# Optimization experiments

Measured on AMD Instinct MI355X. Metric: run time of the kernel, lower is better.

## Reference

```python
import jax, jax.numpy as jnp
import numpy as np

N = 100000      # nodes
E = 1600000     # edges (avg degree 16)
F_IN = 256
F_OUT = 128


def setup_inputs() -> dict:
    key = jax.random.key(0)
    k1, k2, k3, k4, k5 = jax.random.split(key, 5)
    x = jax.random.normal(k1, (N, F_IN), dtype=jnp.float32)
    adj_row = jax.random.randint(k2, (E,), 0, N, dtype=jnp.int32)
    adj_col = jax.random.randint(k3, (E,), 0, N, dtype=jnp.int32)
    adj_vals = jax.random.uniform(k4, (E,), dtype=jnp.float32)
    # he_uniform init for weight, zeros for bias (as in build())
    limit = jnp.sqrt(6.0 / F_IN)
    w = jax.random.uniform(k5, (F_IN, F_OUT), minval=-limit, maxval=limit, dtype=jnp.float32)
    b = jnp.zeros((F_OUT,), dtype=jnp.float32)
    return {"x": x, "adj_row": adj_row, "adj_col": adj_col, "adj_vals": adj_vals, "w": w, "b": b}


def reference(x, adj_row, adj_col, adj_vals, w, b):
    # dense feature transform: [N, F_in] @ [F_in, F_out] -> [N, F_out]
    h = x @ w
    # sparse adjacency SpMM (COO): out[r] += vals[e] * h[c] for edge e=(r,c)
    msgs = adj_vals[:, None] * h[adj_col]            # [E, F_out]
    agg = jax.ops.segment_sum(msgs, adj_row, num_segments=N)  # [N, F_out]
    # bias + relu activation
    return jax.nn.relu(agg + b)
```

## Files before the change

kernel.cpp:

```cpp
#include <hip/hip_runtime.h>
#include <hip/hip_bf16.h>
#include <cstdint>
#include <cstddef>

#define N_NODES 100000
#define N_EDGES 1600000
#define F_IN 256
#define F_OUT 128

#define NB 782
#define NBLK 196
#define TILE 8192
#define CAP 4096

typedef __attribute__((ext_vector_type(8))) short short8;
typedef __attribute__((ext_vector_type(4))) float floatx4;

static __device__ __forceinline__ unsigned short f2bf(float f) {
    union { float f; unsigned u; } v; v.f = f;
    unsigned r = v.u + 0x7FFF + ((v.u >> 16) & 1);
    return (unsigned short)(r >> 16);
}

__global__ void prep_w(const float* __restrict__ w, unsigned short* __restrict__ wT) {
    int i = blockIdx.x * 256 + threadIdx.x;
    int k = i >> 7;
    int n = i & 127;
    int g = (k >> 3) ^ (n & 7);
    wT[n * 256 + g * 8 + (k & 7)] = f2bf(w[i]);
}

__global__ __launch_bounds__(256, 2) void gemm_xw(const float* __restrict__ x,
                                                  const unsigned short* __restrict__ wT,
                                                  unsigned short* __restrict__ h) {
    __shared__ __align__(16) unsigned short wlds[128 * 256];
    const int tid = threadIdx.x;
    {
        const floatx4* src = reinterpret_cast<const floatx4*>(wT);
        floatx4* dst = reinterpret_cast<floatx4*>(wlds);
        #pragma unroll
        for (int i = 0; i < 16; i++) dst[tid + i * 256] = src[tid + i * 256];
    }
    __syncthreads();

    const int wave = tid >> 6, lane = tid & 63;
    const int quad = lane >> 4, l16 = lane & 15;
    const int rowbase = blockIdx.x * 256 + wave * 64;

    floatx4 acc[4][8];
    #pragma unroll
    for (int mf = 0; mf < 4; mf++)
        #pragma unroll
        for (int nt = 0; nt < 8; nt++) acc[mf][nt] = (floatx4)0.f;

    #pragma unroll
    for (int ks = 0; ks < 8; ks++) {
        const int k0 = ks * 32 + quad * 8;
        short8 afrag[4];
        #pragma unroll
        for (int mf = 0; mf < 4; mf++) {
            int row = rowbase + mf * 16 + l16;
            if (row >= N_NODES) row = N_NODES - 1;
            const float* xp = x + (size_t)row * F_IN + k0;
            floatx4 x0 = *reinterpret_cast<const floatx4*>(xp);
            floatx4 x1 = *reinterpret_cast<const floatx4*>(xp + 4);
            short8 a;
            a[0] = (short)f2bf(x0[0]); a[1] = (short)f2bf(x0[1]);
            a[2] = (short)f2bf(x0[2]); a[3] = (short)f2bf(x0[3]);
            a[4] = (short)f2bf(x1[0]); a[5] = (short)f2bf(x1[1]);
            a[6] = (short)f2bf(x1[2]); a[7] = (short)f2bf(x1[3]);
            afrag[mf] = a;
        }
        short8 bfrag[8];
        const int gq = ks * 4 + quad;
        #pragma unroll
        for (int nt = 0; nt < 8; nt++) {
            const int n = nt * 16 + l16;
            const int g = gq ^ (n & 7);
            bfrag[nt] = *reinterpret_cast<const short8*>(&wlds[n * 256 + g * 8]);
        }
        #pragma unroll
        for (int mf = 0; mf < 4; mf++)
            #pragma unroll
            for (int nt = 0; nt < 8; nt++)
                acc[mf][nt] = __builtin_amdgcn_mfma_f32_16x16x32_bf16(
                    afrag[mf], bfrag[nt], acc[mf][nt], 0, 0, 0);
    }

    #pragma unroll
    for (int mf = 0; mf < 4; mf++) {
        const int mbase = rowbase + mf * 16 + quad * 4;
        #pragma unroll
        for (int reg = 0; reg < 4; reg++) {
            const int m = mbase + reg;
            if (m < N_NODES) {
                #pragma unroll
                for (int nt = 0; nt < 8; nt++)
                    h[(size_t)m * F_OUT + nt * 16 + l16] = f2bf(acc[mf][nt][reg]);
            }
        }
    }
}

__global__ __launch_bounds__(256) void bucket_hist(const int* __restrict__ row,
                                                   int* __restrict__ bucket_total,
                                                   int* __restrict__ blockbase) {
    __shared__ int hist[NB];
    const int t = threadIdx.x, blk = blockIdx.x;
    for (int i = t; i < NB; i += 256) hist[i] = 0;
    __syncthreads();
    const long tb = (long)blk * TILE;
    #pragma unroll
    for (int c = 0; c < 8; c++) {
        long i0 = tb + c * 1024 + t * 4;
        if (i0 + 4 <= N_EDGES) {
            int4 r = *reinterpret_cast<const int4*>(row + i0);
            atomicAdd(&hist[r.x >> 7], 1); atomicAdd(&hist[r.y >> 7], 1);
            atomicAdd(&hist[r.z >> 7], 1); atomicAdd(&hist[r.w >> 7], 1);
        } else {
            for (long i = i0; i < N_EDGES && i < i0 + 4; i++)
                atomicAdd(&hist[row[i] >> 7], 1);
        }
    }
    __syncthreads();
    for (int bin = t; bin < NB; bin += 256)
        blockbase[bin * NBLK + blk] = atomicAdd(&bucket_total[bin], hist[bin]);
}

__global__ void bucket_scan(const int* __restrict__ bucket_total,
                            int* __restrict__ bucket_base) {
    __shared__ int sm[1024];
    const int t = threadIdx.x;
    int v = (t < NB) ? bucket_total[t] : 0;
    sm[t] = v; __syncthreads();
    for (int off = 1; off < 1024; off <<= 1) {
        int x2 = (t >= off) ? sm[t - off] : 0;
        __syncthreads();
        sm[t] += x2;
        __syncthreads();
    }
    if (t < NB) bucket_base[t] = sm[t] - v;
    if (t == NB - 1) bucket_base[NB] = sm[t];
}

__global__ __launch_bounds__(256) void bucket_scatter(const int* __restrict__ row,
                                                      const int* __restrict__ col,
                                                      const float* __restrict__ val,
                                                      const int* __restrict__ bucket_base,
                                                      const int* __restrict__ blockbase,
                                                      int2* __restrict__ metabuf) {
    __shared__ int sbase[NB];
    const int t = threadIdx.x, blk = blockIdx.x;
    for (int bin = t; bin < NB; bin += 256)
        sbase[bin] = bucket_base[bin] + blockbase[bin * NBLK + blk];
    __syncthreads();
    const long tb = (long)blk * TILE;
    #pragma unroll
    for (int c = 0; c < 8; c++) {
        long i0 = tb + c * 1024 + t * 4;
        if (i0 + 4 <= N_EDGES) {
            int4 r  = *reinterpret_cast<const int4*>(row + i0);
            int4 cc = *reinterpret_cast<const int4*>(col + i0);
            floatx4 vv = *reinterpret_cast<const floatx4*>(val + i0);
            int rr[4] = {r.x, r.y, r.z, r.w};
            int c4[4] = {cc.x, cc.y, cc.z, cc.w};
            float v4[4] = {vv[0], vv[1], vv[2], vv[3]};
            #pragma unroll
            for (int j = 0; j < 4; j++) {
                int bin = rr[j] >> 7, rl = rr[j] & 127;
                int pos = atomicAdd(&sbase[bin], 1);
                metabuf[pos] = make_int2(c4[j] | (rl << 24), __float_as_int(v4[j]));
            }
        } else {
            for (long i = i0; i < N_EDGES && i < i0 + 4; i++) {
                int rv = row[i];
                int bin = rv >> 7, rl = rv & 127;
                int pos = atomicAdd(&sbase[bin], 1);
                metabuf[pos] = make_int2(col[i] | (rl << 24), __float_as_int(val[i]));
            }
        }
    }
}

__global__ __launch_bounds__(512, 8) void spmm_fused(const unsigned short* __restrict__ h,
                                                     const int* __restrict__ bucket_base,
                                                     const int2* __restrict__ meta,
                                                     const float* __restrict__ bias,
                                                     float* __restrict__ out) {
    __shared__ int2 st[CAP];
    __shared__ int hist[128], scanb[128], startS[128], cursor[128];
    const int t = threadIdx.x, b = blockIdx.x;
    const int b0 = bucket_base[b];
    int n = bucket_base[b + 1] - b0; if (n > CAP) n = CAP;

    if (t < 128) hist[t] = 0;
    __syncthreads();
    for (int i = t; i < n; i += 512)
        atomicAdd(&hist[((unsigned)meta[b0 + i].x >> 24) & 127], 1);
    __syncthreads();
    if (t < 128) scanb[t] = hist[t];
    __syncthreads();
    for (int off = 1; off < 128; off <<= 1) {
        int v = (t >= off && t < 128) ? scanb[t - off] : 0;
        __syncthreads();
        if (t < 128) scanb[t] += v;
        __syncthreads();
    }
    if (t < 128) { int e = scanb[t] - hist[t]; startS[t] = e; cursor[t] = e; }
    __syncthreads();
    for (int i = t; i < n; i += 512) {
        int2 e = meta[b0 + i];
        int rl = ((unsigned)e.x >> 24) & 127;
        int pos = atomicAdd(&cursor[rl], 1);
        st[pos] = make_int2(e.x & 0x00FFFFFF, e.y);
    }
    __syncthreads();

    const int lane = t & 63;
    const int l16 = lane & 15;
    const int grp = (t >> 6) * 4 + (lane >> 4);
    const unsigned short* hp = h + l16 * 8;
    const floatx4 bv0 = *reinterpret_cast<const floatx4*>(bias + l16 * 8);
    const floatx4 bv1 = *reinterpret_cast<const floatx4*>(bias + l16 * 8 + 4);

    #pragma unroll
    for (int j = 0; j < 4; j++) {
        const int rl = grp * 4 + j;
        const int s = startS[rl], d = hist[rl];
        float acc[8];
        #pragma unroll
        for (int k = 0; k < 8; k++) acc[k] = 0.f;
        for (int i = 0; i < d; i += 4) {
            int2 mm[4];
            #pragma unroll
            for (int u = 0; u < 4; u++) {
                int idx = i + u; if (idx > d - 1) idx = d - 1;
                mm[u] = st[s + idx];
            }
            uint4 hv[4];
            #pragma unroll
            for (int u = 0; u < 4; u++)
                hv[u] = *reinterpret_cast<const uint4*>(hp + (size_t)mm[u].x * F_OUT);
            #pragma unroll
            for (int u = 0; u < 4; u++) {
                float v = (i + u < d) ? __int_as_float(mm[u].y) : 0.f;
                #pragma unroll
                for (int k = 0; k < 4; k++) {
                    unsigned uu = ((const unsigned*)&hv[u])[k];
                    acc[2 * k]     += v * __uint_as_float(uu << 16);
                    acc[2 * k + 1] += v * __uint_as_float(uu & 0xffff0000u);
                }
            }
        }
        const int r = b * 128 + rl;
        if (r < N_NODES) {
            floatx4 o0, o1;
            #pragma unroll
            for (int k = 0; k < 4; k++) o0[k] = fmaxf(acc[k] + bv0[k], 0.f);
            #pragma unroll
            for (int k = 0; k < 4; k++) o1[k] = fmaxf(acc[4 + k] + bv1[k], 0.f);
            float* op = out + (size_t)r * F_OUT + l16 * 8;
            *reinterpret_cast<floatx4*>(op) = o0;
            *reinterpret_cast<floatx4*>(op + 4) = o1;
        }
    }
}

extern "C" void kernel_launch(void* const* d_in, const int* in_sizes, int n_in,
                              void* d_out, int out_size, void* d_ws, size_t ws_size,
                              hipStream_t stream) {
    const float* x        = (const float*)d_in[0];
    const int*   adj_row  = (const int*)d_in[1];
    const int*   adj_col  = (const int*)d_in[2];
    const float* adj_vals = (const float*)d_in[3];
    const float* w        = (const float*)d_in[4];
    const float* b        = (const float*)d_in[5];
    float* out = (float*)d_out;

    char* ws = (char*)d_ws;
    unsigned short* wT = (unsigned short*)ws;
    unsigned short* h  = (unsigned short*)(ws + 65536);
    size_t off = 65536 + (size_t)N_NODES * F_OUT * 2;
    int2* metabuf  = (int2*)(ws + off);   off += (size_t)N_EDGES * 8;
    int* blockbase = (int*)(ws + off);    off += (size_t)NB * NBLK * 4;
    int* bucket_total = (int*)(ws + off); off += 3136;
    int* bucket_base  = (int*)(ws + off); off += 3136;

    prep_w<<<128, 256, 0, stream>>>(w, wT);
    hipMemsetAsync(bucket_total, 0, NB * 4, stream);
    gemm_xw<<<(N_NODES + 255) / 256, 256, 0, stream>>>(x, wT, h);
    bucket_hist<<<NBLK, 256, 0, stream>>>(adj_row, bucket_total, blockbase);
    bucket_scan<<<1, 1024, 0, stream>>>(bucket_total, bucket_base);
    bucket_scatter<<<NBLK, 256, 0, stream>>>(adj_row, adj_col, adj_vals,
                                             bucket_base, blockbase, metabuf);
    spmm_fused<<<NB, 512, 0, stream>>>(h, bucket_base, metabuf, b, out);
}
```

Measured before the change: 305.8 us.

## Vectorize h stores, use wave-shuffle scans, and prefetch SpMM gathers

The GEMM now writes each row's eight bf16 outputs as one 16-byte store, so h is kept in a column-interleaved layout. SpMM un-permutes that layout when it writes its output, using strided scalar stores and per-element bias loads. Both prefix scans, the global bucket scan and the per-block row-histogram scan, are replaced by 64-lane shuffle scans, which removes many barriers. The SpMM gather loop is software-pipelined: the next four neighbour rows are loaded while the current four are accumulated, at the cost of higher register pressure.

```diff
diff --git a/kernel.cpp b/kernel.cpp
--- a/kernel.cpp
+++ b/kernel.cpp
@@ -94,9 +94,10 @@
         for (int reg = 0; reg < 4; reg++) {
             const int m = mbase + reg;
             if (m < N_NODES) {
+                short8 hv;
                 #pragma unroll
-                for (int nt = 0; nt < 8; nt++)
-                    h[(size_t)m * F_OUT + nt * 16 + l16] = f2bf(acc[mf][nt][reg]);
+                for (int nt = 0; nt < 8; nt++) hv[nt] = (short)f2bf(acc[mf][nt][reg]);
+                *reinterpret_cast<short8*>(&h[(size_t)m * F_OUT + l16 * 8]) = hv;
             }
         }
     }
@@ -129,18 +130,27 @@
 
 __global__ void bucket_scan(const int* __restrict__ bucket_total,
                             int* __restrict__ bucket_base) {
-    __shared__ int sm[1024];
-    const int t = threadIdx.x;
-    int v = (t < NB) ? bucket_total[t] : 0;
-    sm[t] = v; __syncthreads();
-    for (int off = 1; off < 1024; off <<= 1) {
-        int x2 = (t >= off) ? sm[t - off] : 0;
-        __syncthreads();
-        sm[t] += x2;
-        __syncthreads();
-    }
-    if (t < NB) bucket_base[t] = sm[t] - v;
-    if (t == NB - 1) bucket_base[NB] = sm[t];
+    const int lane = threadIdx.x;
+    int loc[13];
+    int s = 0;
+    #pragma unroll
+    for (int k = 0; k < 13; k++) {
+        int idx = lane * 13 + k;
+        int v = (idx < NB) ? bucket_total[idx] : 0;
+        loc[k] = s; s += v;
+    }
+    int run = s;
+    #pragma unroll
+    for (int off = 1; off < 64; off <<= 1) {
+        int u = __shfl_up(run, off);
+        if (lane >= off) run += u;
+    }
+    const int base = run - s;
+    #pragma unroll
+    for (int k = 0; k < 13; k++) {
+        int idx = lane * 13 + k;
+        if (idx <= NB) bucket_base[idx] = base + loc[k];
+    }
 }
 
 __global__ __launch_bounds__(256) void bucket_scatter(const int* __restrict__ row,
@@ -188,7 +198,7 @@
                                                      const float* __restrict__ bias,
                                                      float* __restrict__ out) {
     __shared__ int2 st[CAP];
-    __shared__ int hist[128], scanb[128], startS[128], cursor[128];
+    __shared__ int hist[128], startS[128], cursor[128];
     const int t = threadIdx.x, b = blockIdx.x;
     const int b0 = bucket_base[b];
     int n = bucket_base[b + 1] - b0; if (n > CAP) n = CAP;
@@ -198,15 +208,19 @@
     for (int i = t; i < n; i += 512)
         atomicAdd(&hist[((unsigned)meta[b0 + i].x >> 24) & 127], 1);
     __syncthreads();
-    if (t < 128) scanb[t] = hist[t];
-    __syncthreads();
-    for (int off = 1; off < 128; off <<= 1) {
-        int v = (t >= off && t < 128) ? scanb[t - off] : 0;
-        __syncthreads();
-        if (t < 128) scanb[t] += v;
-        __syncthreads();
-    }
-    if (t < 128) { int e = scanb[t] - hist[t]; startS[t] = e; cursor[t] = e; }
+    if (t < 64) {
+        int h0 = hist[t], h1 = hist[t + 64];
+        int s0 = h0, s1 = h1;
+        #pragma unroll
+        for (int off = 1; off < 64; off <<= 1) {
+            int u0 = __shfl_up(s0, off);
+            int u1 = __shfl_up(s1, off);
+            if (t >= off) { s0 += u0; s1 += u1; }
+        }
+        s1 += __shfl(s0, 63);
+        startS[t] = s0 - h0;      cursor[t] = s0 - h0;
+        startS[t + 64] = s1 - h1; cursor[t + 64] = s1 - h1;
+    }
     __syncthreads();
     for (int i = t; i < n; i += 512) {
         int2 e = meta[b0 + i];
@@ -220,8 +234,6 @@
     const int l16 = lane & 15;
     const int grp = (t >> 6) * 4 + (lane >> 4);
     const unsigned short* hp = h + l16 * 8;
-    const floatx4 bv0 = *reinterpret_cast<const floatx4*>(bias + l16 * 8);
-    const floatx4 bv1 = *reinterpret_cast<const floatx4*>(bias + l16 * 8 + 4);
 
     #pragma unroll
     for (int j = 0; j < 4; j++) {
@@ -230,38 +242,52 @@
         float acc[8];
         #pragma unroll
         for (int k = 0; k < 8; k++) acc[k] = 0.f;
-        for (int i = 0; i < d; i += 4) {
-            int2 mm[4];
-            #pragma unroll
-            for (int u = 0; u < 4; u++) {
-                int idx = i + u; if (idx > d - 1) idx = d - 1;
-                mm[u] = st[s + idx];
-            }
-            uint4 hv[4];
+        if (d > 0) {
+            int2 mmc[4];
+            uint4 hvc[4];
+            #pragma unroll
+            for (int u = 0; u < 4; u++) { int idx = (u < d) ? u : d - 1; mmc[u] = st[s + idx]; }
             #pragma unroll
             for (int u = 0; u < 4; u++)
-                hv[u] = *reinterpret_cast<const uint4*>(hp + (size_t)mm[u].x * F_OUT);
-            #pragma unroll
-            for (int u = 0; u < 4; u++) {
-                float v = (i + u < d) ? __int_as_float(mm[u].y) : 0.f;
+                hvc[u] = *reinterpret_cast<const uint4*>(hp + (size_t)mmc[u].x * F_OUT);
+            for (int i = 0; i < d; i += 4) {
+                int2 mmn[4];
+                uint4 hvn[4];
+                const bool more = (i + 4) < d;
+                if (more) {
+                    #pragma unroll
+                    for (int u = 0; u < 4; u++) {
+                        int idx = i + 4 + u; if (idx > d - 1) idx = d - 1;
+                        mmn[u] = st[s + idx];
+                    }
+                    #pragma unroll
+                    for (int u = 0; u < 4; u++)
+                        hvn[u] = *reinterpret_cast<const uint4*>(hp + (size_t)mmn[u].x * F_OUT);
+                }
                 #pragma unroll
-                for (int k = 0; k < 4; k++) {
-                    unsigned uu = ((const unsigned*)&hv[u])[k];
-                    acc[2 * k]     += v * __uint_as_float(uu << 16);
-                    acc[2 * k + 1] += v * __uint_as_float(uu & 0xffff0000u);
+                for (int u = 0; u < 4; u++) {
+                    float v = (i + u < d) ? __int_as_float(mmc[u].y) : 0.f;
+                    #pragma unroll
+                    for (int k = 0; k < 4; k++) {
+                        unsigned uu = ((const unsigned*)&hvc[u])[k];
+                        acc[2 * k]     += v * __uint_as_float(uu << 16);
+                        acc[2 * k + 1] += v * __uint_as_float(uu & 0xffff0000u);
+                    }
+                }
+                if (more) {
+                    #pragma unroll
+                    for (int u = 0; u < 4; u++) { mmc[u] = mmn[u]; hvc[u] = hvn[u]; }
                 }
             }
         }
         const int r = b * 128 + rl;
         if (r < N_NODES) {
-            floatx4 o0, o1;
-            #pragma unroll
-            for (int k = 0; k < 4; k++) o0[k] = fmaxf(acc[k] + bv0[k], 0.f);
-            #pragma unroll
-            for (int k = 0; k < 4; k++) o1[k] = fmaxf(acc[4 + k] + bv1[k], 0.f);
-            float* op = out + (size_t)r * F_OUT + l16 * 8;
-            *reinterpret_cast<floatx4*>(op) = o0;
-            *reinterpret_cast<floatx4*>(op + 4) = o1;
+            float* op = out + (size_t)r * F_OUT + l16;
+            #pragma unroll
+            for (int jc = 0; jc < 8; jc++) {
+                float o = fmaxf(acc[jc] + bias[jc * 16 + l16], 0.f);
+                op[jc * 16] = o;
+            }
         }
     }
 }
@@ -290,7 +316,7 @@
     hipMemsetAsync(bucket_total, 0, NB * 4, stream);
     gemm_xw<<<(N_NODES + 255) / 256, 256, 0, stream>>>(x, wT, h);
     bucket_hist<<<NBLK, 256, 0, stream>>>(adj_row, bucket_total, blockbase);
-    bucket_scan<<<1, 1024, 0, stream>>>(bucket_total, bucket_base);
+    bucket_scan<<<1, 64, 0, stream>>>(bucket_total, bucket_base);
     bucket_scatter<<<NBLK, 256, 0, stream>>>(adj_row, adj_col, adj_vals,
                                              bucket_base, blockbase, metabuf);
     spmm_fused<<<NB, 512, 0, stream>>>(h, bucket_base, metabuf, b, out);
```

Result: slower. 467.1 us (+52.8%).
